# Kernel tuning notes

Hardware: AMD Instinct MI355X
Metric: run time of the kernel (lower is better)

Reference implementation:

```python
import jax, jax.numpy as jnp
import numpy as np


def setup_inputs() -> dict:
    key = jax.random.key(0)
    k1, k2, k3 = jax.random.split(key, 3)
    B, T, D = 2, 2048, 1024
    x = jax.random.normal(k1, (B, T, D), dtype=jnp.float32)
    w_qkv = jax.random.normal(k2, (3 * D, D), dtype=jnp.float32) * (D ** -0.5)
    w_out = jax.random.normal(k3, (D, D), dtype=jnp.float32) * (D ** -0.5)
    return {"x": x, "w_qkv": w_qkv, "w_out": w_out, "heads": 16}


def reference(x, w_qkv, w_out, heads):
    # SelfAttention forward: attention_type='sdp', position_mode='alibi', causal=True, eval mode.
    B, T, D = x.shape
    H = heads
    hd = D // H
    scale = hd ** -0.5

    # qkv projection: torch Linear -> x @ W^T
    qkv = (x @ w_qkv.T).reshape(B, T, 3, H, hd)
    qkv = jnp.transpose(qkv, (2, 0, 3, 1, 4))  # [3, B, H, T, hd]
    q, k, v = qkv[0], qkv[1], qkv[2]

    # ALiBi relative bias: slopes = 1 / 2^(h/H) for h = 1..H
    slopes = 1.0 / jnp.power(2.0, jnp.arange(1, H + 1, dtype=jnp.float32) / H)
    pos = jnp.arange(T, dtype=jnp.float32)
    rel = jnp.abs(pos[:, None] - pos[None, :])  # [T, T]
    bias = -slopes[None, :, None, None] * rel[None, None, :, :]  # [1, H, T, T]

    # scores + causal mask + softmax (manual path since position_bias is not None)
    scores = jnp.einsum('bhqd,bhkd->bhqk', q, k) * scale + bias
    causal_mask = jnp.triu(jnp.ones((T, T), dtype=bool), k=1)
    scores = jnp.where(causal_mask[None, None, :, :], -jnp.inf, scores)
    attn = jax.nn.softmax(scores, axis=-1)
    attn = jnp.where(jnp.isnan(attn), 1.0 / float(max(T, 1)), attn)

    out = jnp.einsum('bhqk,bhkd->bhqd', attn, v)  # [B, H, T, hd]
    out = jnp.transpose(out, (0, 2, 1, 3)).reshape(B, T, D)
    return out @ w_out.T
```

## Files before the change

kernel.cpp:

```cpp
#include <hip/hip_runtime.h>
#include <hip/hip_bf16.h>

typedef __attribute__((ext_vector_type(8))) short shortx8;
typedef __attribute__((ext_vector_type(4))) float floatx4;
typedef __attribute__((ext_vector_type(16))) float floatx16;
typedef __attribute__((ext_vector_type(4))) unsigned uintx4;
typedef __attribute__((ext_vector_type(2))) unsigned uintx2;

#define B_ 2
#define T_ 2048
#define D_ 1024
#define H_ 16
#define HD_ 64
#define SCALE 0.125f
#define QSCALE 0.18033688011112042f
#define SMAX2 23.083120654223414f
#define FULLH ((size_t)B_ * H_ * T_ * HD_)

#define GLDS16(g, l) __builtin_amdgcn_global_load_lds( \
    (__attribute__((address_space(1))) void*)(g), \
    (__attribute__((address_space(3))) void*)(l), 16, 0, 0)

__device__ __forceinline__ short f2bf(float f) {
    union { float f; unsigned u; } v; v.f = f;
    unsigned r = v.u + 0x7FFFu + ((v.u >> 16) & 1u);
    return (short)(r >> 16);
}

__device__ __forceinline__ unsigned pk2(float x, float y) {
    union { __hip_bfloat162 h; unsigned u; } t;
    t.h = __float22bfloat162_rn(make_float2(x, y));
    return t.u;
}

__device__ __forceinline__ shortx8 cvt8(floatx4 a, floatx4 b) {
    uintx4 r = { pk2(a[0], a[1]), pk2(a[2], a[3]), pk2(b[0], b[1]), pk2(b[2], b[3]) };
    return __builtin_bit_cast(shortx8, r);
}

__device__ __forceinline__ float ex2(float x) {
#if __has_builtin(__builtin_amdgcn_exp2f)
    return __builtin_amdgcn_exp2f(x);
#else
    return exp2f(x);
#endif
}

__global__ __launch_bounds__(256) void cvt_xw(const float* __restrict__ x,
                                              const float* __restrict__ wqkv,
                                              short* __restrict__ xbf,
                                              short* __restrict__ wbf) {
    int i = blockIdx.x * 256 + threadIdx.x;
    const float* src; short* dst; int o;
    if (i < 524288) { src = x; dst = xbf; o = i; }
    else            { src = wqkv; dst = wbf; o = i - 524288; }
    const floatx4* p = reinterpret_cast<const floatx4*>(src) + (size_t)o * 2;
    *(reinterpret_cast<shortx8*>(dst) + o) = cvt8(p[0], p[1]);
}

__global__ __launch_bounds__(256) void qkv_fast(const short* __restrict__ xbf,
                                                const short* __restrict__ wbf,
                                                short* __restrict__ qout,
                                                short* __restrict__ kv) {
    __shared__ __align__(16) short As[128 * 64];
    __shared__ __align__(16) short Bs[128 * 64];

    const int tid = threadIdx.x;
    const int wv = tid >> 6;
    const int l  = tid & 63;
    const int ln = l & 15;
    const int quad = l >> 4;
    const int rowb = quad << 2;
    const int wm = wv >> 1, wn = wv & 1;

    const int id  = blockIdx.x;
    const int xcd = id & 7;
    const int tt  = id >> 3;
    const int bx  = xcd * 3 + (tt >> 5);
    const int by  = tt & 31;
    const int m0 = by * 128;
    const int n0g = bx * 128;

    const int lr = l >> 3, lc = l & 7;
    const int gcol = (lc ^ lr) << 3;
    const short* agp = xbf + (size_t)(m0 + wv * 32 + lr) * D_ + gcol;
    const short* bgp = wbf + (size_t)(n0g + wv * 32 + lr) * D_ + gcol;
    short* aldsb = As + wv * 32 * 64;
    short* bldsb = Bs + wv * 32 * 64;

    floatx4 acc[4][4] = {};

    for (int k0 = 0; k0 < D_; k0 += 64) {
        __syncthreads();
#pragma unroll
        for (int c = 0; c < 4; ++c) {
            GLDS16(agp + (size_t)(c * 8) * D_ + k0, aldsb + c * 512);
            GLDS16(bgp + (size_t)(c * 8) * D_ + k0, bldsb + c * 512);
        }
        __syncthreads();

#pragma unroll
        for (int kk = 0; kk < 2; ++kk) {
            const int csw = (kk << 2) + quad;
            const int sw = (csw ^ (ln & 7)) << 3;
            shortx8 af[4], bf[4];
#pragma unroll
            for (int i = 0; i < 4; ++i)
                af[i] = *reinterpret_cast<const shortx8*>(&As[((wm * 64 + i * 16 + ln) << 6) + sw]);
#pragma unroll
            for (int j = 0; j < 4; ++j)
                bf[j] = *reinterpret_cast<const shortx8*>(&Bs[((wn * 64 + j * 16 + ln) << 6) + sw]);
#pragma unroll
            for (int i = 0; i < 4; ++i)
#pragma unroll
                for (int j = 0; j < 4; ++j)
                    acc[i][j] = __builtin_amdgcn_mfma_f32_16x16x32_bf16(af[i], bf[j], acc[i][j], 0, 0, 0);
        }
    }

    const int sel = n0g >> 10;
    const int bb = m0 >> 11;
    const int t0w = (m0 + wm * 64) & (T_ - 1);
    const int h = ((n0g + wn * 64) >> 6) & 15;

    if (sel < 2) {
        short* dst = (sel == 0) ? qout : kv;
        const float sc = (sel == 0) ? QSCALE : 1.0f;
        const size_t hb = (size_t)(bb * H_ + h) * T_;
#pragma unroll
        for (int i = 0; i < 4; ++i)
#pragma unroll
            for (int r = 0; r < 4; ++r) {
                int t = t0w + i * 16 + rowb + r;
#pragma unroll
                for (int j = 0; j < 4; ++j)
                    dst[(hb + t) * HD_ + j * 16 + ln] = f2bf(acc[i][j][r] * sc);
            }
    } else {
        __syncthreads();
        short* tb = (wv < 2) ? (As + wv * 4096) : (Bs + (wv - 2) * 4096);
        short* vhead = kv + FULLH + (size_t)(bb * H_ + h) * HD_ * T_;
        const int dl = l & 31, th = (l >> 5) << 5;
#pragma unroll
        for (int p = 0; p < 2; ++p) {
#pragma unroll
            for (int i = 0; i < 4; ++i)
#pragma unroll
                for (int jj = 0; jj < 2; ++jj) {
                    int j = 2 * p + jj;
#pragma unroll
                    for (int r = 0; r < 4; ++r)
                        tb[(jj * 16 + ln) * 72 + i * 16 + rowb + r] = f2bf(acc[i][j][r]);
                }
            short* vd = vhead + (size_t)(p * 32 + dl) * T_ + t0w + th;
#pragma unroll
            for (int seg = 0; seg < 4; ++seg)
                *reinterpret_cast<shortx8*>(vd + seg * 8) =
                    *reinterpret_cast<const shortx8*>(&tb[dl * 72 + th + seg * 8]);
        }
    }
}

__global__ __launch_bounds__(256) void out_fast(const short* __restrict__ Abf,
                                                const short* __restrict__ wbf,
                                                float* __restrict__ out) {
    __shared__ __align__(16) short As[64 * 64];
    __shared__ __align__(16) short Bs[128 * 64];

    const int tid = threadIdx.x;
    const int wv = tid >> 6;
    const int l  = tid & 63;
    const int ln = l & 15;
    const int quad = l >> 4;
    const int rowb = quad << 2;
    const int wm = wv >> 1, wn = wv & 1;

    const int id = blockIdx.x;
    const int m0 = (id >> 3) * 64;
    const int n0g = (id & 7) * 128;

    const int lr = l >> 3, lc = l & 7;
    const int gcol = (lc ^ lr) << 3;
    const short* bgp = wbf + (size_t)(n0g + wv * 32 + lr) * D_ + gcol;
    short* aldsb = As + wv * 16 * 64;
    short* bldsb = Bs + wv * 32 * 64;

    size_t abase[2];
#pragma unroll
    for (int c = 0; c < 2; ++c) {
        int m = m0 + wv * 16 + c * 8 + lr;
        int bb2 = m >> 11, t = m & (T_ - 1);
        abase[c] = ((size_t)(bb2 * H_) * T_ + t) * HD_ + gcol;
    }

    floatx4 acc[2][4] = {};

    for (int k0 = 0; k0 < D_; k0 += 64) {
        const size_t hoff = (size_t)(k0 >> 6) * T_ * HD_;
        __syncthreads();
#pragma unroll
        for (int c = 0; c < 2; ++c)
            GLDS16(Abf + abase[c] + hoff, aldsb + c * 512);
#pragma unroll
        for (int c = 0; c < 4; ++c)
            GLDS16(bgp + (size_t)(c * 8) * D_ + k0, bldsb + c * 512);
        __syncthreads();

#pragma unroll
        for (int kk = 0; kk < 2; ++kk) {
            const int csw = (kk << 2) + quad;
            const int sw = (csw ^ (ln & 7)) << 3;
            shortx8 af[2], bf[4];
#pragma unroll
            for (int i = 0; i < 2; ++i)
                af[i] = *reinterpret_cast<const shortx8*>(&As[((wm * 32 + i * 16 + ln) << 6) + sw]);
#pragma unroll
            for (int j = 0; j < 4; ++j)
                bf[j] = *reinterpret_cast<const shortx8*>(&Bs[((wn * 64 + j * 16 + ln) << 6) + sw]);
#pragma unroll
            for (int i = 0; i < 2; ++i)
#pragma unroll
                for (int j = 0; j < 4; ++j)
                    acc[i][j] = __builtin_amdgcn_mfma_f32_16x16x32_bf16(af[i], bf[j], acc[i][j], 0, 0, 0);
        }
    }

#pragma unroll
    for (int i = 0; i < 2; ++i)
#pragma unroll
        for (int r = 0; r < 4; ++r) {
            int m = m0 + wm * 32 + i * 16 + rowb + r;
#pragma unroll
            for (int j = 0; j < 4; ++j)
                out[(size_t)m * D_ + n0g + wn * 64 + j * 16 + ln] = acc[i][j][r];
        }
}

__global__ __launch_bounds__(128, 2) void attn(const short* __restrict__ qws,
                                               const short* __restrict__ kv,
                                               short* ao,
                                               const float* __restrict__ wout,
                                               short* __restrict__ wobf) {
    if (blockIdx.x >= 1024) {
        int i = (blockIdx.x - 1024) * 128 + threadIdx.x;
        const floatx4* p = reinterpret_cast<const floatx4*>(wout) + (size_t)i * 2;
        *(reinterpret_cast<shortx8*>(wobf) + i) = cvt8(p[0], p[1]);
        return;
    }

    __shared__ __align__(16) short Ks[64 * 64];
    __shared__ __align__(16) short Vt[64 * 64];

    const int tid = threadIdx.x;
    const int wv = tid >> 6;
    const int l  = tid & 63;
    const int ql = l & 31;
    const int hi = l >> 5;

    const int id  = blockIdx.x;
    const int xcd = id & 7;
    const int u2  = (id >> 3) & 3;
    const int rr  = (id >> 5) & 7;
    const int tt  = id >> 8;
    const int bh  = xcd * 4 + u2;
    const int qblk = (tt == 0) ? 31 - rr : (tt == 1) ? rr : (tt == 2) ? 23 - rr : 8 + rr;
    const int h = bh & 15, b = bh >> 4;

    const float slope2 = 1.4426950408889634f * exp2f(-(float)(h + 1) * 0.0625f);
    const size_t koff = (size_t)(b * H_ + h) * T_ * HD_;
    const int q0w = qblk * 64 + wv * 32;

    shortx8 qf[4];
#pragma unroll
    for (int ds = 0; ds < 4; ++ds)
        qf[ds] = *reinterpret_cast<const shortx8*>(&qws[koff + (size_t)(q0w + ql) * HD_ + ds * 16 + hi * 8]);

    const float cbase = slope2 * (float)(4 * hi - (q0w + ql)) - SMAX2;
    float rb[16];
#pragma unroll
    for (int g = 0; g < 16; ++g)
        rb[g] = cbase + slope2 * (float)((g & 3) + 8 * (g >> 2));
    const float s32 = slope2 * 32.0f;

    const int lr = l >> 3, lc = l & 7;
    const int gcol = (lc ^ lr) << 3;
    const short* kgp = kv + koff + (size_t)(wv * 32 + lr) * HD_ + gcol;
    const short* vgp = kv + FULLH + koff + (size_t)(wv * 32 + lr) * T_ + gcol;
    short* klds = Ks + wv * 32 * 64;
    short* vlds = Vt + wv * 32 * 64;

    const int qs7 = ql & 7;

    floatx16 o0 = {}, o1 = {}, ls = {};
    const shortx8 ones = {16256, 16256, 16256, 16256, 16256, 16256, 16256, 16256};
    const int qlh = ql - 4 * hi;

    for (int kb = 0; kb <= qblk; ++kb) {
        __syncthreads();
#pragma unroll
        for (int c = 0; c < 4; ++c) {
            GLDS16(kgp + (size_t)(kb * 64 + c * 8) * HD_, klds + c * 512);
            GLDS16(vgp + (size_t)(c * 8) * T_ + kb * 64, vlds + c * 512);
        }
        __syncthreads();

        const bool diag = (kb == qblk);
        const float tb = slope2 * (float)(kb * 64);

#pragma unroll
        for (int nc = 0; nc < 2; ++nc) {
            const bool act = !diag || (nc == 0) || (wv == 1);
            if (!act) continue;
            const bool part = diag && (nc == wv);

            floatx16 sacc = {};
#pragma unroll
            for (int ds = 0; ds < 4; ++ds) {
                const int kcol = ((ds * 2 + hi) ^ qs7) << 3;
                shortx8 kf = *reinterpret_cast<const shortx8*>(&Ks[((nc * 32 + ql) << 6) + kcol]);
                sacc = __builtin_amdgcn_mfma_f32_32x32x16_bf16(kf, qf[ds], sacc, 0, 0, 0);
            }

            const float tnc = tb + (nc ? s32 : 0.0f);
            float p[16];
#pragma unroll
            for (int g = 0; g < 16; ++g) {
                float ev = ex2(sacc[g] + (rb[g] + tnc));
                if (part) {
                    const int kc2 = (g & 3) + 8 * (g >> 2);
                    ev = (kc2 <= qlh) ? ev : 0.0f;
                }
                p[g] = ev;
            }

            unsigned cv[4][2];
#pragma unroll
            for (int g = 0; g < 4; ++g) {
                cv[g][0] = pk2(p[4 * g + 0], p[4 * g + 1]);
                cv[g][1] = pk2(p[4 * g + 2], p[4 * g + 3]);
            }

            __builtin_amdgcn_s_setprio(1);
#pragma unroll
            for (int kh = 0; kh < 2; ++kh) {
                unsigned w0 = cv[2 * kh][0], w2 = cv[2 * kh + 1][0];
                unsigned w1 = cv[2 * kh][1], w3 = cv[2 * kh + 1][1];
                asm volatile("v_permlane32_swap_b32 %0, %1" : "+v"(w0), "+v"(w2));
                asm volatile("v_permlane32_swap_b32 %0, %1" : "+v"(w1), "+v"(w3));
                uintx4 uu = {w0, w1, w2, w3};
                shortx8 apv = __builtin_bit_cast(shortx8, uu);
                const int ks = nc * 2 + kh;
                const int vcol = ((ks * 2 + hi) ^ qs7) << 3;
                ls = __builtin_amdgcn_mfma_f32_32x32x16_bf16(apv, ones, ls, 0, 0, 0);
                shortx8 vf0 = *reinterpret_cast<const shortx8*>(&Vt[(ql << 6) + vcol]);
                o0 = __builtin_amdgcn_mfma_f32_32x32x16_bf16(apv, vf0, o0, 0, 0, 0);
                shortx8 vf1 = *reinterpret_cast<const shortx8*>(&Vt[((32 + ql) << 6) + vcol]);
                o1 = __builtin_amdgcn_mfma_f32_32x32x16_bf16(apv, vf1, o1, 0, 0, 0);
            }
            __builtin_amdgcn_s_setprio(0);
        }
    }

#pragma unroll
    for (int g = 0; g < 16; ++g) {
        const int qrow = (g & 3) + 8 * (g >> 2) + 4 * hi;
        const float inv = 1.0f / ls[g];
        const size_t ob = koff + (size_t)(q0w + qrow) * HD_ + ql;
        ao[ob]      = f2bf(o0[g] * inv);
        ao[ob + 32] = f2bf(o1[g] * inv);
    }
}

__global__ __launch_bounds__(256) void qkv_slow(const float* __restrict__ x,
                                                const float* __restrict__ wqkv,
                                                short* __restrict__ qout,
                                                short* __restrict__ kv) {
    __shared__ __align__(16) short As[64][72];
    __shared__ __align__(16) short Bs[64][72];
    const int tid = threadIdx.x;
    const int wv = tid >> 6, l = tid & 63, ln = l & 15, quad = l >> 4, qd = quad << 3;
    const int m0 = blockIdx.y * 64;
    const int sel = blockIdx.x >> 4, h = blockIdx.x & 15;
    const int nrow = sel * D_ + h * HD_;
    const int sr0 = tid >> 3, sc0 = (tid & 7) << 3, sr1 = sr0 + 32;
    floatx4 fa[4], fb[4];
    auto FETCH = [&](int k0) {
        const float* ap = &x[(size_t)(m0 + sr0) * D_ + k0 + sc0];
        fa[0] = *reinterpret_cast<const floatx4*>(ap);
        fa[1] = *reinterpret_cast<const floatx4*>(ap + 4);
        ap += (size_t)32 * D_;
        fa[2] = *reinterpret_cast<const floatx4*>(ap);
        fa[3] = *reinterpret_cast<const floatx4*>(ap + 4);
        const float* bp = &wqkv[(size_t)(nrow + sr0) * D_ + k0 + sc0];
        fb[0] = *reinterpret_cast<const floatx4*>(bp);
        fb[1] = *reinterpret_cast<const floatx4*>(bp + 4);
        bp += (size_t)32 * D_;
        fb[2] = *reinterpret_cast<const floatx4*>(bp);
        fb[3] = *reinterpret_cast<const floatx4*>(bp + 4);
    };
    floatx4 acc[4] = {};
    FETCH(0);
    for (int k0 = 0; k0 < D_; k0 += 64) {
        __syncthreads();
        *reinterpret_cast<shortx8*>(&As[sr0][sc0]) = cvt8(fa[0], fa[1]);
        *reinterpret_cast<shortx8*>(&As[sr1][sc0]) = cvt8(fa[2], fa[3]);
        *reinterpret_cast<shortx8*>(&Bs[sr0][sc0]) = cvt8(fb[0], fb[1]);
        *reinterpret_cast<shortx8*>(&Bs[sr1][sc0]) = cvt8(fb[2], fb[3]);
        __syncthreads();
        if (k0 + 64 < D_) FETCH(k0 + 64);
        const int mr = (wv << 4) + ln;
#pragma unroll
        for (int kk = 0; kk < 2; ++kk) {
            shortx8 a = *reinterpret_cast<const shortx8*>(&As[mr][kk * 32 + qd]);
#pragma unroll
            for (int nc = 0; nc < 4; ++nc) {
                shortx8 bq = *reinterpret_cast<const shortx8*>(&Bs[nc * 16 + ln][kk * 32 + qd]);
                acc[nc] = __builtin_amdgcn_mfma_f32_16x16x32_bf16(a, bq, acc[nc], 0, 0, 0);
            }
        }
    }
    const int bb = m0 >> 11, t0 = m0 & (T_ - 1);
    if (sel < 2) {
        short* dst = (sel == 0) ? qout : kv;
        const float sc = (sel == 0) ? QSCALE : 1.0f;
#pragma unroll
        for (int r = 0; r < 4; ++r) {
            int t = t0 + (wv << 4) + (quad << 2) + r;
#pragma unroll
            for (int nc = 0; nc < 4; ++nc)
                dst[((size_t)(bb * H_ + h) * T_ + t) * HD_ + nc * 16 + ln] = f2bf(acc[nc][r] * sc);
        }
    } else {
        __syncthreads();
#pragma unroll
        for (int r = 0; r < 4; ++r)
#pragma unroll
            for (int nc = 0; nc < 4; ++nc)
                As[nc * 16 + ln][(wv << 4) + (quad << 2) + r] = f2bf(acc[nc][r]);
        __syncthreads();
        const int d = tid >> 2, tseg = (tid & 3) << 4;
        short* vdst = kv + FULLH + ((size_t)(bb * H_ + h) * HD_ + d) * T_ + t0 + tseg;
        *reinterpret_cast<shortx8*>(vdst)     = *reinterpret_cast<const shortx8*>(&As[d][tseg]);
        *reinterpret_cast<shortx8*>(vdst + 8) = *reinterpret_cast<const shortx8*>(&As[d][tseg + 8]);
    }
}

__global__ __launch_bounds__(256) void out_slow(const short* __restrict__ A,
                                                const float* __restrict__ W,
                                                float* __restrict__ out) {
    __shared__ __align__(16) short As[64][72];
    __shared__ __align__(16) short Bs[64][72];
    const int tid = threadIdx.x;
    const int wv = tid >> 6, l = tid & 63, ln = l & 15, quad = l >> 4, qd = quad << 3;
    const int m0 = blockIdx.y * 64, n0 = blockIdx.x * 64;
    const int sr0 = tid >> 3, sc0 = (tid & 7) << 3, sr1 = sr0 + 32;
    shortx8 sa0, sa1;
    floatx4 fb[4];
    auto FETCH = [&](int k0) {
        const int h = k0 >> 6;
        int m = m0 + sr0;
        int bb = m >> 11, t = m & (T_ - 1);
        sa0 = *reinterpret_cast<const shortx8*>(A + ((size_t)(bb * H_ + h) * T_ + t) * HD_ + sc0);
        m = m0 + sr1; bb = m >> 11; t = m & (T_ - 1);
        sa1 = *reinterpret_cast<const shortx8*>(A + ((size_t)(bb * H_ + h) * T_ + t) * HD_ + sc0);
        const float* bp = &W[(size_t)(n0 + sr0) * D_ + k0 + sc0];
        fb[0] = *reinterpret_cast<const floatx4*>(bp);
        fb[1] = *reinterpret_cast<const floatx4*>(bp + 4);
        bp += (size_t)32 * D_;
        fb[2] = *reinterpret_cast<const floatx4*>(bp);
        fb[3] = *reinterpret_cast<const floatx4*>(bp + 4);
    };
    floatx4 acc[4] = {};
    FETCH(0);
    for (int k0 = 0; k0 < D_; k0 += 64) {
        __syncthreads();
        *reinterpret_cast<shortx8*>(&As[sr0][sc0]) = sa0;
        *reinterpret_cast<shortx8*>(&As[sr1][sc0]) = sa1;
        *reinterpret_cast<shortx8*>(&Bs[sr0][sc0]) = cvt8(fb[0], fb[1]);
        *reinterpret_cast<shortx8*>(&Bs[sr1][sc0]) = cvt8(fb[2], fb[3]);
        __syncthreads();
        if (k0 + 64 < D_) FETCH(k0 + 64);
        const int mr = (wv << 4) + ln;
#pragma unroll
        for (int kk = 0; kk < 2; ++kk) {
            shortx8 a = *reinterpret_cast<const shortx8*>(&As[mr][kk * 32 + qd]);
#pragma unroll
            for (int nc = 0; nc < 4; ++nc) {
                shortx8 bq = *reinterpret_cast<const shortx8*>(&Bs[nc * 16 + ln][kk * 32 + qd]);
                acc[nc] = __builtin_amdgcn_mfma_f32_16x16x32_bf16(a, bq, acc[nc], 0, 0, 0);
            }
        }
    }
#pragma unroll
    for (int r = 0; r < 4; ++r) {
        int m = m0 + (wv << 4) + (quad << 2) + r;
#pragma unroll
        for (int nc = 0; nc < 4; ++nc)
            out[(size_t)m * D_ + n0 + nc * 16 + ln] = acc[nc][r];
    }
}

extern "C" void kernel_launch(void* const* d_in, const int* in_sizes, int n_in,
                              void* d_out, int out_size, void* d_ws, size_t ws_size,
                              hipStream_t stream) {
    const float* x    = (const float*)d_in[0];
    const float* wqkv = (const float*)d_in[1];
    const float* wout = (const float*)d_in[2];

    short* kvbuf = (short*)d_out;
    float* out   = (float*)d_out;

    if (ws_size >= 23068672ULL) {
        short* xbf  = (short*)d_ws;
        short* wbf  = xbf + 4 * 1024 * 1024;
        short* qws  = xbf + 7 * 1024 * 1024;
        short* wobf = xbf;

        cvt_xw<<<3584, 256, 0, stream>>>(x, wqkv, xbf, wbf);
        qkv_fast<<<dim3(768), 256, 0, stream>>>(xbf, wbf, qws, kvbuf);
        attn<<<dim3(2048), 128, 0, stream>>>(qws, kvbuf, qws, wout, wobf);
        out_fast<<<dim3(512), 256, 0, stream>>>(qws, wobf, out);
    } else {
        short* qws = (short*)d_ws;
        qkv_slow<<<dim3(48, 64), 256, 0, stream>>>(x, wqkv, qws, kvbuf);
        attn<<<dim3(1024), 128, 0, stream>>>(qws, kvbuf, qws, nullptr, nullptr);
        out_slow<<<dim3(16, 64), 256, 0, stream>>>(qws, wout, out);
    }
}
```

Before: 184.1 us.

## Double-buffer K/V tiles via register prefetch in attention kernel

```diff
diff --git a/kernel.cpp b/kernel.cpp
--- a/kernel.cpp
+++ b/kernel.cpp
@@ -248,8 +248,8 @@
         return;
     }
 
-    __shared__ __align__(16) short Ks[64 * 64];
-    __shared__ __align__(16) short Vt[64 * 64];
+    __shared__ __align__(16) short Ks[2][64][72];
+    __shared__ __align__(16) short Vt[2][64][72];
 
     const int tid = threadIdx.x;
     const int wv = tid >> 6;
@@ -269,6 +269,7 @@
     const float slope2 = 1.4426950408889634f * exp2f(-(float)(h + 1) * 0.0625f);
     const size_t koff = (size_t)(b * H_ + h) * T_ * HD_;
     const int q0w = qblk * 64 + wv * 32;
+    const int e = qblk + 1;
 
     shortx8 qf[4];
 #pragma unroll
@@ -282,27 +283,43 @@
         rb[g] = cbase + slope2 * (float)((g & 3) + 8 * (g >> 2));
     const float s32 = slope2 * 32.0f;
 
-    const int lr = l >> 3, lc = l & 7;
-    const int gcol = (lc ^ lr) << 3;
-    const short* kgp = kv + koff + (size_t)(wv * 32 + lr) * HD_ + gcol;
-    const short* vgp = kv + FULLH + koff + (size_t)(wv * 32 + lr) * T_ + gcol;
-    short* klds = Ks + wv * 32 * 64;
-    short* vlds = Vt + wv * 32 * 64;
-
-    const int qs7 = ql & 7;
+    const int sr = tid >> 1;
+    const int sc = (tid & 1) << 5;
+    const short* kbase = kv + koff;
+    const short* vbase = kv + FULLH + koff;
+    shortx8 kR[4], vR[4];
+    auto FETCH = [&](int kb) {
+        const short* kp = kbase + (((size_t)(kb * 64 + sr)) << 6) + sc;
+        const short* vp = vbase + (size_t)sr * T_ + kb * 64 + sc;
+#pragma unroll
+        for (int s = 0; s < 4; ++s) {
+            kR[s] = *reinterpret_cast<const shortx8*>(kp + 8 * s);
+            vR[s] = *reinterpret_cast<const shortx8*>(vp + 8 * s);
+        }
+    };
+    auto STAGE = [&](int bi) {
+#pragma unroll
+        for (int s = 0; s < 4; ++s) {
+            *reinterpret_cast<shortx8*>(&Ks[bi][sr][sc + 8 * s]) = kR[s];
+            *reinterpret_cast<shortx8*>(&Vt[bi][sr][sc + 8 * s]) = vR[s];
+        }
+    };
 
     floatx16 o0 = {}, o1 = {}, ls = {};
     const shortx8 ones = {16256, 16256, 16256, 16256, 16256, 16256, 16256, 16256};
     const int qlh = ql - 4 * hi;
 
-    for (int kb = 0; kb <= qblk; ++kb) {
-        __syncthreads();
-#pragma unroll
-        for (int c = 0; c < 4; ++c) {
-            GLDS16(kgp + (size_t)(kb * 64 + c * 8) * HD_, klds + c * 512);
-            GLDS16(vgp + (size_t)(c * 8) * T_ + kb * 64, vlds + c * 512);
-        }
-        __syncthreads();
+    FETCH(0);
+    STAGE(0);
+    if (e > 1) FETCH(1);
+    __syncthreads();
+
+    for (int kb = 0; kb < e; ++kb) {
+        const int cur = kb & 1;
+        if (kb + 1 < e) {
+            STAGE(cur ^ 1);
+            if (kb + 2 < e) FETCH(kb + 2);
+        }
 
         const bool diag = (kb == qblk);
         const float tb = slope2 * (float)(kb * 64);
@@ -316,8 +333,7 @@
             floatx16 sacc = {};
 #pragma unroll
             for (int ds = 0; ds < 4; ++ds) {
-                const int kcol = ((ds * 2 + hi) ^ qs7) << 3;
-                shortx8 kf = *reinterpret_cast<const shortx8*>(&Ks[((nc * 32 + ql) << 6) + kcol]);
+                shortx8 kf = *reinterpret_cast<const shortx8*>(&Ks[cur][nc * 32 + ql][ds * 16 + hi * 8]);
                 sacc = __builtin_amdgcn_mfma_f32_32x32x16_bf16(kf, qf[ds], sacc, 0, 0, 0);
             }
 
@@ -350,15 +366,15 @@
                 uintx4 uu = {w0, w1, w2, w3};
                 shortx8 apv = __builtin_bit_cast(shortx8, uu);
                 const int ks = nc * 2 + kh;
-                const int vcol = ((ks * 2 + hi) ^ qs7) << 3;
                 ls = __builtin_amdgcn_mfma_f32_32x32x16_bf16(apv, ones, ls, 0, 0, 0);
-                shortx8 vf0 = *reinterpret_cast<const shortx8*>(&Vt[(ql << 6) + vcol]);
+                shortx8 vf0 = *reinterpret_cast<const shortx8*>(&Vt[cur][ql][ks * 16 + hi * 8]);
                 o0 = __builtin_amdgcn_mfma_f32_32x32x16_bf16(apv, vf0, o0, 0, 0, 0);
-                shortx8 vf1 = *reinterpret_cast<const shortx8*>(&Vt[((32 + ql) << 6) + vcol]);
+                shortx8 vf1 = *reinterpret_cast<const shortx8*>(&Vt[cur][32 + ql][ks * 16 + hi * 8]);
                 o1 = __builtin_amdgcn_mfma_f32_32x32x16_bf16(apv, vf1, o1, 0, 0, 0);
             }
             __builtin_amdgcn_s_setprio(0);
         }
+        __syncthreads();
     }
 
 #pragma unroll
```

After: 181.4 us. About the same (-1.5%).
